# Kernel tuning notes

Hardware: AMD Instinct MI355X
Metric: run time of the kernel (lower is better)

## Reference

```python
import jax, jax.numpy as jnp
import numpy as np

K = 10          # number of clusters (static; matches randint fill_max)
ALPHA = 0.02    # intra-cluster margin
DELTA = 0.5     # inter-cluster margin
LAMBDA_INTRA = 1.0
LAMBDA_INTER = 1.0
MIN_WEIGHT = 50.0


def setup_inputs() -> dict:
    key = jax.random.key(0)
    k1, k2 = jax.random.split(key)
    x = jax.random.normal(k1, (8, 64, 240, 320), dtype=jnp.float32)
    # module assumes NORMALIZED unit vectors along channel dim
    x = x / jnp.maximum(jnp.linalg.norm(x, axis=1, keepdims=True), 1e-12)
    cluster_masks = jax.random.randint(k2, (8, 1, 240, 320), 0, K, dtype=jnp.int32)
    return {"x": x, "cluster_masks": cluster_masks}


def reference(x, cluster_masks):
    B, C, H, W = x.shape
    cm = cluster_masks[:, 0]  # (B, H, W) int
    # one-hot cluster assignment; out-of-range ids (e.g. -1 = unlabeled) -> all zeros
    onehot = jax.nn.one_hot(cm, K, dtype=x.dtype)  # (B, H, W, K)

    # ---- spherical cluster means (fused segment-reduce over H*W) ----
    sums = jnp.einsum('bchw,bhwk->bck', x, onehot)          # (B, C, K)
    counts = jnp.sum(onehot, axis=(1, 2))                    # (B, K)
    means = sums / (counts[:, None, :] + 1e-10)
    # F.normalize(p=2, dim=1): x / max(||x||, eps)
    means = means / jnp.maximum(jnp.linalg.norm(means, axis=1, keepdims=True), 1e-12)

    # ---- broadcast means back to pixels ----
    tiled = jnp.einsum('bck,bhwk->bchw', means, onehot)      # (B, C, H, W)

    labeled = (cm >= 0).astype(x.dtype)                      # (B, H, W)
    # cosine metric
    intra_d = labeled * (0.5 * (1.0 - jnp.sum(x * tiled, axis=1)))  # (B, H, W)

    # ---- per-cluster hard-example weighting ----
    indicator = (intra_d > ALPHA).astype(x.dtype)            # (B, H, W)
    N_k = jnp.einsum('bhw,bhwk->bk', indicator, onehot)      # (B, K)
    weights = jnp.einsum('bk,bhwk->bhw', N_k, onehot)        # (B, H, W)
    weights = jnp.maximum(weights, MIN_WEIGHT) * K
    intra_loss = jnp.sum(intra_d ** 2 / weights) / B
    intra_loss = LAMBDA_INTRA * jnp.where(jnp.sum(indicator) > 0, intra_loss, 0.0)

    # ---- inter-cluster hinge loss (K > 1 statically) ----
    inter_d = 0.5 * (1.0 - jnp.einsum('bck,bcl->bkl', means, means))  # (B, K, K)
    hinge = jnp.maximum(DELTA - inter_d, 0.0) * (1.0 - jnp.eye(K, dtype=x.dtype))
    inter_loss = LAMBDA_INTER * jnp.sum(hinge ** 2) / (K * (K - 1) / 2 * B)

    loss = intra_loss + inter_loss
    return (loss, intra_loss, inter_loss)
```

## Files before the change

### kernel.cpp

```cpp
#include <hip/hip_runtime.h>
#include <hip/hip_bf16.h>

#define B_ 8
#define C_ 64
#define H_ 240
#define W_ 320
#define HW_ (H_ * W_)
#define HW4_ (HW_ / 4)
#define K_ 10
#define ALPHA_ 0.02f
#define DELTA_ 0.5f
#define MIN_WEIGHT_ 50.0f

#define K1_SPLIT 8


__global__ __launch_bounds__(256) void k1_sums(
    const float* __restrict__ x, const int* __restrict__ cm,
    float* __restrict__ sums, float* __restrict__ counts) {
  const int c = blockIdx.x;
  const int b = blockIdx.y;
  const int z = blockIdx.z;
  const int tid = threadIdx.x;

  const int chunk = HW4_ / K1_SPLIT;
  const int lo = z * chunk;
  const int hi = lo + chunk;

  const float4* __restrict__ xp =
      (const float4*)(x + (size_t)(b * C_ + c) * HW_);
  const int4* __restrict__ cp = (const int4*)(cm + (size_t)b * HW_);

  float acc[K_];
#pragma unroll
  for (int j = 0; j < K_; ++j) acc[j] = 0.f;
  float cnt[K_];
#pragma unroll
  for (int j = 0; j < K_; ++j) cnt[j] = 0.f;
  const bool do_cnt = (c == 0);

  for (int i = lo + tid; i < hi; i += 256) {
    float4 v = xp[i];
    int4 k4 = cp[i];
#pragma unroll
    for (int j = 0; j < K_; ++j) {
      acc[j] += (k4.x == j ? v.x : 0.f);
      acc[j] += (k4.y == j ? v.y : 0.f);
      acc[j] += (k4.z == j ? v.z : 0.f);
      acc[j] += (k4.w == j ? v.w : 0.f);
    }
    if (do_cnt) {
#pragma unroll
      for (int j = 0; j < K_; ++j) {
        cnt[j] += (float)((k4.x == j) + (k4.y == j) + (k4.z == j) + (k4.w == j));
      }
    }
  }

#pragma unroll
  for (int j = 0; j < K_; ++j) {
    float v = acc[j];
#pragma unroll
    for (int off = 32; off > 0; off >>= 1) v += __shfl_down(v, off, 64);
    if ((tid & 63) == 0) atomicAdd(&sums[(b * C_ + c) * K_ + j], v);
  }
  if (do_cnt) {
#pragma unroll
    for (int j = 0; j < K_; ++j) {
      float v = cnt[j];
#pragma unroll
      for (int off = 32; off > 0; off >>= 1) v += __shfl_down(v, off, 64);
      if ((tid & 63) == 0) atomicAdd(&counts[b * K_ + j], v);
    }
  }
}

__global__ __launch_bounds__(256) void k3_intra(
    const float* __restrict__ x, const int* __restrict__ cm,
    const float* __restrict__ sums, const float* __restrict__ counts,
    float* __restrict__ means, float* __restrict__ S2,
    float* __restrict__ Nk, float* __restrict__ indtot) {
  const int b = blockIdx.y;
  const int chunk = blockIdx.x;
  const int tid = threadIdx.x;
  const int lane_p = tid & 63;
  const int grp = tid >> 6;

  __shared__ float mlds[C_ * K_];
  __shared__ float nrm[K_];
  __shared__ float4 pd[256];
  __shared__ float s2b[K_];
  __shared__ float nkb[K_];

  for (int i = tid; i < C_ * K_; i += 256) {
    const int k = i % K_;
    mlds[i] = sums[b * C_ * K_ + i] / (counts[b * K_ + k] + 1e-10f);
  }
  if (tid < K_) { s2b[tid] = 0.f; nkb[tid] = 0.f; }
  __syncthreads();
  if (tid < K_) {
    float n2 = 0.f;
#pragma unroll
    for (int c = 0; c < C_; ++c) {
      const float mm = mlds[c * K_ + tid];
      n2 += mm * mm;
    }
    nrm[tid] = 1.f / fmaxf(sqrtf(n2), 1e-12f);
  }
  __syncthreads();
  for (int i = tid; i < C_ * K_; i += 256) mlds[i] *= nrm[i % K_];
  __syncthreads();
  if (chunk == 0) {
    for (int i = tid; i < C_ * K_; i += 256) means[b * C_ * K_ + i] = mlds[i];
  }

  const int p4 = chunk * 64 + lane_p;
  const int4 k4 = ((const int4*)(cm + (size_t)b * HW_))[p4];
  const float4* __restrict__ xb = (const float4*)(x + (size_t)b * C_ * HW_);

  float d0 = 0.f, d1 = 0.f, d2 = 0.f, d3 = 0.f;
  const int c0 = grp * (C_ / 4);
#pragma unroll
  for (int cc = 0; cc < C_ / 4; ++cc) {
    const int c = c0 + cc;
    float4 v = xb[c * HW4_ + p4];
    const float* mr = &mlds[c * K_];
    d0 += v.x * mr[k4.x];
    d1 += v.y * mr[k4.y];
    d2 += v.z * mr[k4.z];
    d3 += v.w * mr[k4.w];
  }
  pd[tid] = make_float4(d0, d1, d2, d3);
  __syncthreads();

  if (grp == 0) {
    float4 a = pd[lane_p];
    float4 bb = pd[lane_p + 64];
    float4 cc = pd[lane_p + 128];
    float4 dd = pd[lane_p + 192];
    const float i0 = 0.5f * (1.f - (a.x + bb.x + cc.x + dd.x));
    const float i1 = 0.5f * (1.f - (a.y + bb.y + cc.y + dd.y));
    const float i2 = 0.5f * (1.f - (a.z + bb.z + cc.z + dd.z));
    const float i3 = 0.5f * (1.f - (a.w + bb.w + cc.w + dd.w));

    atomicAdd(&s2b[k4.x], i0 * i0);
    atomicAdd(&s2b[k4.y], i1 * i1);
    atomicAdd(&s2b[k4.z], i2 * i2);
    atomicAdd(&s2b[k4.w], i3 * i3);
    atomicAdd(&nkb[k4.x], i0 > ALPHA_ ? 1.f : 0.f);
    atomicAdd(&nkb[k4.y], i1 > ALPHA_ ? 1.f : 0.f);
    atomicAdd(&nkb[k4.z], i2 > ALPHA_ ? 1.f : 0.f);
    atomicAdd(&nkb[k4.w], i3 > ALPHA_ ? 1.f : 0.f);
  }
  __syncthreads();

  if (tid < K_) {
    atomicAdd(&S2[b * K_ + tid], s2b[tid]);
    atomicAdd(&Nk[b * K_ + tid], nkb[tid]);
    atomicAdd(indtot, nkb[tid]);
  }
}

__global__ __launch_bounds__(256) void k4_final(
    const float* __restrict__ means, const float* __restrict__ S2,
    const float* __restrict__ Nk, const float* __restrict__ indtot,
    float* __restrict__ out) {
  const int tid = threadIdx.x;

  float h2 = 0.f;
  for (int t = tid; t < B_ * 45; t += 256) {
    const int b = t / 45;
    int idx = t % 45;
    int k = 0, l = 0;
    for (k = 0; k < K_; ++k) {
      const int row = K_ - 1 - k;
      if (idx < row) { l = k + 1 + idx; break; }
      idx -= row;
    }
    float g = 0.f;
    for (int c = 0; c < C_; ++c)
      g += means[(b * C_ + c) * K_ + k] * means[(b * C_ + c) * K_ + l];
    const float inter_d = 0.5f * (1.f - g);
    const float h = fmaxf(DELTA_ - inter_d, 0.f);
    h2 += 2.f * h * h;
  }

  __shared__ float red[256];
  red[tid] = h2;
  __syncthreads();
  for (int s = 128; s > 0; s >>= 1) {
    if (tid < s) red[tid] += red[tid + s];
    __syncthreads();
  }
  if (tid == 0) {
    const float inter = red[0] / (float)((K_ * (K_ - 1) / 2) * B_);
    float intra = 0.f;
    for (int i = 0; i < B_ * K_; ++i) {
      const float w = fmaxf(Nk[i], MIN_WEIGHT_) * (float)K_;
      intra += S2[i] / w;
    }
    intra /= (float)B_;
    if (!(indtot[0] > 0.f)) intra = 0.f;
    out[0] = intra + inter;
    out[1] = intra;
    out[2] = inter;
  }
}

extern "C" void kernel_launch(void* const* d_in, const int* in_sizes, int n_in,
                              void* d_out, int out_size, void* d_ws, size_t ws_size,
                              hipStream_t stream) {
  const float* x = (const float*)d_in[0];
  const int* cm = (const int*)d_in[1];

  float* ws = (float*)d_ws;
  float* sums = ws;
  float* counts = ws + 5120;
  float* means = ws + 5200;
  float* S2 = ws + 10320;
  float* Nk = ws + 10400;
  float* indtot = ws + 10480;

  hipMemsetAsync(d_ws, 0, 10481 * sizeof(float), stream);

  k1_sums<<<dim3(C_, B_, K1_SPLIT), 256, 0, stream>>>(x, cm, sums, counts);
  k3_intra<<<dim3(HW4_ / 64, B_), 256, 0, stream>>>(x, cm, sums, counts, means,
                                                    S2, Nk, indtot);
  k4_final<<<1, 256, 0, stream>>>(means, S2, Nk, indtot, (float*)d_out);
}
```

Baseline: 295.6 us.

## Fuse three kernels into one persistent kernel with grid-wide atomic barriers

Replaces the sums, intra-distance and final kernels with a single persistent kernel of 1024 blocks that synchronises through atomic grid barriers in workspace. This removes two kernel launches and their gaps, and block 0 performs the final reduction after the second barrier. The first phase uses 2 blocks per (b,c) plane instead of 8, and the second phase loops over larger pixel chunks per block. The design depends on all 1024 blocks being co-resident (launch bounds of 4 blocks per CU), otherwise the barrier deadlocks. The 20KB shared buffer for all means also limits occupancy.

```diff
diff --git a/kernel.cpp b/kernel.cpp
--- a/kernel.cpp
+++ b/kernel.cpp
@@ -12,160 +12,200 @@
 #define DELTA_ 0.5f
 #define MIN_WEIGHT_ 50.0f
 
-#define K1_SPLIT 8
-
-
-__global__ __launch_bounds__(256) void k1_sums(
+#define NBLK 1024
+#define SCOPE_AGENT __HIP_MEMORY_SCOPE_AGENT
+
+
+__device__ inline float wave_red(float v) {
+#pragma unroll
+  for (int off = 32; off > 0; off >>= 1) v += __shfl_down(v, off, 64);
+  return v;
+}
+
+__device__ inline void grid_barrier(unsigned* bar, int tid, bool wait) {
+  __syncthreads();
+  if (tid == 0) {
+    __hip_atomic_fetch_add(bar, 1u, __ATOMIC_ACQ_REL, SCOPE_AGENT);
+    if (wait) {
+      while (__hip_atomic_load(bar, __ATOMIC_ACQUIRE, SCOPE_AGENT) < NBLK)
+        __builtin_amdgcn_s_sleep(8);
+    }
+  }
+  __syncthreads();
+}
+
+__device__ inline float aload(const float* p) {
+  return __hip_atomic_load(p, __ATOMIC_RELAXED, SCOPE_AGENT);
+}
+
+__global__ __launch_bounds__(256, 4) void fused(
     const float* __restrict__ x, const int* __restrict__ cm,
-    float* __restrict__ sums, float* __restrict__ counts) {
-  const int c = blockIdx.x;
-  const int b = blockIdx.y;
-  const int z = blockIdx.z;
+    float* __restrict__ ws, float* __restrict__ out) {
+  float* sums = ws;
+  float* counts = ws + 5120;
+  float* means = ws + 5200;
+  float* S2 = ws + 10320;
+  float* Nk = ws + 10400;
+  float* indtot = ws + 10480;
+  unsigned* bar1 = (unsigned*)(ws + 10488);
+  unsigned* bar2 = (unsigned*)(ws + 10489);
+
+  const int blk = blockIdx.x;
   const int tid = threadIdx.x;
 
-  const int chunk = HW4_ / K1_SPLIT;
-  const int lo = z * chunk;
-  const int hi = lo + chunk;
-
-  const float4* __restrict__ xp =
-      (const float4*)(x + (size_t)(b * C_ + c) * HW_);
-  const int4* __restrict__ cp = (const int4*)(cm + (size_t)b * HW_);
-
-  float acc[K_];
-#pragma unroll
-  for (int j = 0; j < K_; ++j) acc[j] = 0.f;
-  float cnt[K_];
-#pragma unroll
-  for (int j = 0; j < K_; ++j) cnt[j] = 0.f;
-  const bool do_cnt = (c == 0);
-
-  for (int i = lo + tid; i < hi; i += 256) {
-    float4 v = xp[i];
-    int4 k4 = cp[i];
-#pragma unroll
-    for (int j = 0; j < K_; ++j) {
-      acc[j] += (k4.x == j ? v.x : 0.f);
-      acc[j] += (k4.y == j ? v.y : 0.f);
-      acc[j] += (k4.z == j ? v.z : 0.f);
-      acc[j] += (k4.w == j ? v.w : 0.f);
-    }
-    if (do_cnt) {
-#pragma unroll
-      for (int j = 0; j < K_; ++j) {
-        cnt[j] += (float)((k4.x == j) + (k4.y == j) + (k4.z == j) + (k4.w == j));
-      }
-    }
-  }
-
-#pragma unroll
-  for (int j = 0; j < K_; ++j) {
-    float v = acc[j];
-#pragma unroll
-    for (int off = 32; off > 0; off >>= 1) v += __shfl_down(v, off, 64);
-    if ((tid & 63) == 0) atomicAdd(&sums[(b * C_ + c) * K_ + j], v);
-  }
-  if (do_cnt) {
-#pragma unroll
-    for (int j = 0; j < K_; ++j) {
-      float v = cnt[j];
-#pragma unroll
-      for (int off = 32; off > 0; off >>= 1) v += __shfl_down(v, off, 64);
-      if ((tid & 63) == 0) atomicAdd(&counts[b * K_ + j], v);
-    }
-  }
-}
-
-__global__ __launch_bounds__(256) void k3_intra(
-    const float* __restrict__ x, const int* __restrict__ cm,
-    const float* __restrict__ sums, const float* __restrict__ counts,
-    float* __restrict__ means, float* __restrict__ S2,
-    float* __restrict__ Nk, float* __restrict__ indtot) {
-  const int b = blockIdx.y;
-  const int chunk = blockIdx.x;
-  const int tid = threadIdx.x;
-  const int lane_p = tid & 63;
-  const int grp = tid >> 6;
-
   __shared__ float mlds[C_ * K_];
+  __shared__ float cl[K_];
   __shared__ float nrm[K_];
   __shared__ float4 pd[256];
   __shared__ float s2b[K_];
   __shared__ float nkb[K_];
-
-  for (int i = tid; i < C_ * K_; i += 256) {
-    const int k = i % K_;
-    mlds[i] = sums[b * C_ * K_ + i] / (counts[b * K_ + k] + 1e-10f);
-  }
-  if (tid < K_) { s2b[tid] = 0.f; nkb[tid] = 0.f; }
-  __syncthreads();
-  if (tid < K_) {
-    float n2 = 0.f;
-#pragma unroll
-    for (int c = 0; c < C_; ++c) {
-      const float mm = mlds[c * K_ + tid];
-      n2 += mm * mm;
-    }
-    nrm[tid] = 1.f / fmaxf(sqrtf(n2), 1e-12f);
-  }
-  __syncthreads();
-  for (int i = tid; i < C_ * K_; i += 256) mlds[i] *= nrm[i % K_];
-  __syncthreads();
-  if (chunk == 0) {
-    for (int i = tid; i < C_ * K_; i += 256) means[b * C_ * K_ + i] = mlds[i];
-  }
-
-  const int p4 = chunk * 64 + lane_p;
-  const int4 k4 = ((const int4*)(cm + (size_t)b * HW_))[p4];
-  const float4* __restrict__ xb = (const float4*)(x + (size_t)b * C_ * HW_);
-
-  float d0 = 0.f, d1 = 0.f, d2 = 0.f, d3 = 0.f;
-  const int c0 = grp * (C_ / 4);
-#pragma unroll
-  for (int cc = 0; cc < C_ / 4; ++cc) {
-    const int c = c0 + cc;
-    float4 v = xb[c * HW4_ + p4];
-    const float* mr = &mlds[c * K_];
-    d0 += v.x * mr[k4.x];
-    d1 += v.y * mr[k4.y];
-    d2 += v.z * mr[k4.z];
-    d3 += v.w * mr[k4.w];
-  }
-  pd[tid] = make_float4(d0, d1, d2, d3);
-  __syncthreads();
-
-  if (grp == 0) {
-    float4 a = pd[lane_p];
-    float4 bb = pd[lane_p + 64];
-    float4 cc = pd[lane_p + 128];
-    float4 dd = pd[lane_p + 192];
-    const float i0 = 0.5f * (1.f - (a.x + bb.x + cc.x + dd.x));
-    const float i1 = 0.5f * (1.f - (a.y + bb.y + cc.y + dd.y));
-    const float i2 = 0.5f * (1.f - (a.z + bb.z + cc.z + dd.z));
-    const float i3 = 0.5f * (1.f - (a.w + bb.w + cc.w + dd.w));
-
-    atomicAdd(&s2b[k4.x], i0 * i0);
-    atomicAdd(&s2b[k4.y], i1 * i1);
-    atomicAdd(&s2b[k4.z], i2 * i2);
-    atomicAdd(&s2b[k4.w], i3 * i3);
-    atomicAdd(&nkb[k4.x], i0 > ALPHA_ ? 1.f : 0.f);
-    atomicAdd(&nkb[k4.y], i1 > ALPHA_ ? 1.f : 0.f);
-    atomicAdd(&nkb[k4.z], i2 > ALPHA_ ? 1.f : 0.f);
-    atomicAdd(&nkb[k4.w], i3 > ALPHA_ ? 1.f : 0.f);
-  }
-  __syncthreads();
-
-  if (tid < K_) {
-    atomicAdd(&S2[b * K_ + tid], s2b[tid]);
-    atomicAdd(&Nk[b * K_ + tid], nkb[tid]);
-    atomicAdd(indtot, nkb[tid]);
-  }
-}
-
-__global__ __launch_bounds__(256) void k4_final(
-    const float* __restrict__ means, const float* __restrict__ S2,
-    const float* __restrict__ Nk, const float* __restrict__ indtot,
-    float* __restrict__ out) {
-  const int tid = threadIdx.x;
+  __shared__ float red[256];
+  __shared__ float mall[B_ * C_ * K_];
+
+  {
+    const int plane = blk >> 1;
+    const int half = blk & 1;
+    const int b = plane >> 6;
+    const int c = plane & 63;
+    const float4* __restrict__ xp = (const float4*)(x + (size_t)plane * HW_);
+    const int4* __restrict__ cp = (const int4*)(cm + (size_t)b * HW_);
+
+    float acc[K_];
+#pragma unroll
+    for (int j = 0; j < K_; ++j) acc[j] = 0.f;
+    float cnt[K_];
+#pragma unroll
+    for (int j = 0; j < K_; ++j) cnt[j] = 0.f;
+    const bool do_cnt = (c == 0);
+
+    const int lo = half * (HW4_ / 2);
+    const int hi = lo + (HW4_ / 2);
+#pragma unroll 2
+    for (int i = lo + tid; i < hi; i += 256) {
+      float4 v = xp[i];
+      int4 k4 = cp[i];
+#pragma unroll
+      for (int j = 0; j < K_; ++j) {
+        acc[j] += (k4.x == j ? v.x : 0.f);
+        acc[j] += (k4.y == j ? v.y : 0.f);
+        acc[j] += (k4.z == j ? v.z : 0.f);
+        acc[j] += (k4.w == j ? v.w : 0.f);
+      }
+      if (do_cnt) {
+#pragma unroll
+        for (int j = 0; j < K_; ++j) {
+          cnt[j] += (float)((k4.x == j) + (k4.y == j) + (k4.z == j) + (k4.w == j));
+        }
+      }
+    }
+
+#pragma unroll
+    for (int j = 0; j < K_; ++j) {
+      float v = wave_red(acc[j]);
+      if ((tid & 63) == 0) atomicAdd(&sums[plane * K_ + j], v);
+    }
+    if (do_cnt) {
+#pragma unroll
+      for (int j = 0; j < K_; ++j) {
+        float v = wave_red(cnt[j]);
+        if ((tid & 63) == 0) atomicAdd(&counts[b * K_ + j], v);
+      }
+    }
+  }
+
+  grid_barrier(bar1, tid, true);
+
+  {
+    const int b = blk >> 7;
+    const int chunk = blk & 127;
+
+    if (tid < K_) {
+      cl[tid] = aload(&counts[b * K_ + tid]);
+      s2b[tid] = 0.f;
+      nkb[tid] = 0.f;
+    }
+    __syncthreads();
+    for (int i = tid; i < C_ * K_; i += 256)
+      mlds[i] = aload(&sums[b * C_ * K_ + i]) / (cl[i % K_] + 1e-10f);
+    __syncthreads();
+    if (tid < K_) {
+      float n2 = 0.f;
+#pragma unroll
+      for (int c = 0; c < C_; ++c) {
+        const float mm = mlds[c * K_ + tid];
+        n2 += mm * mm;
+      }
+      nrm[tid] = 1.f / fmaxf(sqrtf(n2), 1e-12f);
+    }
+    __syncthreads();
+    for (int i = tid; i < C_ * K_; i += 256) mlds[i] *= nrm[i % K_];
+    __syncthreads();
+    if (chunk == 0) {
+      for (int i = tid; i < C_ * K_; i += 256)
+        __hip_atomic_store(&means[b * C_ * K_ + i], mlds[i], __ATOMIC_RELAXED,
+                           SCOPE_AGENT);
+    }
+
+    const int lane_p = tid & 63;
+    const int grp = tid >> 6;
+    const int lo = chunk * (HW4_ / 128);
+    const float4* __restrict__ xb = (const float4*)(x + (size_t)b * C_ * HW_);
+    const int4* __restrict__ cp = (const int4*)(cm + (size_t)b * HW_);
+
+    for (int base = 0; base < HW4_ / 128; base += 64) {
+      const int off = base + lane_p;
+      const bool act = off < HW4_ / 128;
+      const int p4 = lo + off;
+      int4 k4 = act ? cp[p4] : make_int4(0, 0, 0, 0);
+      float d0 = 0.f, d1 = 0.f, d2 = 0.f, d3 = 0.f;
+      if (act) {
+        const int c0 = grp * (C_ / 4);
+#pragma unroll
+        for (int cc = 0; cc < C_ / 4; ++cc) {
+          const int c = c0 + cc;
+          float4 v = xb[c * HW4_ + p4];
+          const float* mr = &mlds[c * K_];
+          d0 += v.x * mr[k4.x];
+          d1 += v.y * mr[k4.y];
+          d2 += v.z * mr[k4.z];
+          d3 += v.w * mr[k4.w];
+        }
+      }
+      pd[tid] = make_float4(d0, d1, d2, d3);
+      __syncthreads();
+      if (grp == 0 && act) {
+        float4 a = pd[lane_p];
+        float4 bb = pd[lane_p + 64];
+        float4 cc = pd[lane_p + 128];
+        float4 dd = pd[lane_p + 192];
+        const float i0 = 0.5f * (1.f - (a.x + bb.x + cc.x + dd.x));
+        const float i1 = 0.5f * (1.f - (a.y + bb.y + cc.y + dd.y));
+        const float i2 = 0.5f * (1.f - (a.z + bb.z + cc.z + dd.z));
+        const float i3 = 0.5f * (1.f - (a.w + bb.w + cc.w + dd.w));
+        atomicAdd(&s2b[k4.x], i0 * i0);
+        atomicAdd(&s2b[k4.y], i1 * i1);
+        atomicAdd(&s2b[k4.z], i2 * i2);
+        atomicAdd(&s2b[k4.w], i3 * i3);
+        atomicAdd(&nkb[k4.x], i0 > ALPHA_ ? 1.f : 0.f);
+        atomicAdd(&nkb[k4.y], i1 > ALPHA_ ? 1.f : 0.f);
+        atomicAdd(&nkb[k4.z], i2 > ALPHA_ ? 1.f : 0.f);
+        atomicAdd(&nkb[k4.w], i3 > ALPHA_ ? 1.f : 0.f);
+      }
+      __syncthreads();
+    }
+
+    if (tid < K_) {
+      atomicAdd(&S2[b * K_ + tid], s2b[tid]);
+      atomicAdd(&Nk[b * K_ + tid], nkb[tid]);
+      atomicAdd(indtot, nkb[tid]);
+    }
+  }
+
+  grid_barrier(bar2, tid, blk == 0);
+  if (blk != 0) return;
+
+  for (int i = tid; i < B_ * C_ * K_; i += 256) mall[i] = aload(&means[i]);
+  __syncthreads();
 
   float h2 = 0.f;
   for (int t = tid; t < B_ * 45; t += 256) {
@@ -178,29 +218,37 @@
       idx -= row;
     }
     float g = 0.f;
+#pragma unroll 8
     for (int c = 0; c < C_; ++c)
-      g += means[(b * C_ + c) * K_ + k] * means[(b * C_ + c) * K_ + l];
+      g += mall[(b * C_ + c) * K_ + k] * mall[(b * C_ + c) * K_ + l];
     const float inter_d = 0.5f * (1.f - g);
     const float h = fmaxf(DELTA_ - inter_d, 0.f);
     h2 += 2.f * h * h;
   }
-
-  __shared__ float red[256];
   red[tid] = h2;
   __syncthreads();
   for (int s = 128; s > 0; s >>= 1) {
     if (tid < s) red[tid] += red[tid + s];
     __syncthreads();
   }
+  const float inter = red[0] / (float)((K_ * (K_ - 1) / 2) * B_);
+  __syncthreads();
+
+  float iv = 0.f;
+  if (tid < B_ * K_) {
+    const float s2 = aload(&S2[tid]);
+    const float nk = aload(&Nk[tid]);
+    iv = s2 / (fmaxf(nk, MIN_WEIGHT_) * (float)K_);
+  }
+  red[tid] = iv;
+  __syncthreads();
+  for (int s = 128; s > 0; s >>= 1) {
+    if (tid < s) red[tid] += red[tid + s];
+    __syncthreads();
+  }
   if (tid == 0) {
-    const float inter = red[0] / (float)((K_ * (K_ - 1) / 2) * B_);
-    float intra = 0.f;
-    for (int i = 0; i < B_ * K_; ++i) {
-      const float w = fmaxf(Nk[i], MIN_WEIGHT_) * (float)K_;
-      intra += S2[i] / w;
-    }
-    intra /= (float)B_;
-    if (!(indtot[0] > 0.f)) intra = 0.f;
+    float intra = red[0] / (float)B_;
+    if (!(aload(indtot) > 0.f)) intra = 0.f;
     out[0] = intra + inter;
     out[1] = intra;
     out[2] = inter;
@@ -212,19 +260,9 @@
                               hipStream_t stream) {
   const float* x = (const float*)d_in[0];
   const int* cm = (const int*)d_in[1];
-
   float* ws = (float*)d_ws;
-  float* sums = ws;
-  float* counts = ws + 5120;
-  float* means = ws + 5200;
-  float* S2 = ws + 10320;
-  float* Nk = ws + 10400;
-  float* indtot = ws + 10480;
-
-  hipMemsetAsync(d_ws, 0, 10481 * sizeof(float), stream);
-
-  k1_sums<<<dim3(C_, B_, K1_SPLIT), 256, 0, stream>>>(x, cm, sums, counts);
-  k3_intra<<<dim3(HW4_ / 64, B_), 256, 0, stream>>>(x, cm, sums, counts, means,
-                                                    S2, Nk, indtot);
-  k4_final<<<1, 256, 0, stream>>>(means, S2, Nk, indtot, (float*)d_out);
-}
+
+  hipMemsetAsync(d_ws, 0, 10496 * sizeof(float), stream);
+
+  fused<<<NBLK, 256, 0, stream>>>(x, cm, ws, (float*)d_out);
+}
```

New measurement: 468.9 us. 1.59x slower.
